# Optimization experiments

Measured on AMD Instinct MI355X. Metric: run time of the kernel, lower is better.

The kernel has to match this reference:

```python
import jax, jax.numpy as jnp
import numpy as np

SCALING = 16.0 / 16.0  # lora_alpha / r

def setup_inputs() -> dict:
    key = jax.random.key(0)
    k1, k2, k3, k4, k5 = jax.random.split(key, 5)
    B, S, D, R = 4, 4096, 4096, 16
    x = jax.random.normal(k1, (B, S, D), dtype=jnp.float32)
    W = jax.random.normal(k2, (D, D), dtype=jnp.float32) * (1.0 / np.sqrt(D))
    bias = jax.random.normal(k3, (D,), dtype=jnp.float32) * 0.02
    lora_A = jax.random.normal(k4, (D, R), dtype=jnp.float32) * (1.0 / np.sqrt(D))
    lora_B = jax.random.normal(k5, (R, D), dtype=jnp.float32) * 0.02
    return {"x": x, "W": W, "bias": bias, "lora_A": lora_A, "lora_B": lora_B}

def reference(x, W, bias, lora_A, lora_B):
    x_dtype = x.dtype
    # base (quantized) linear modeled as dense GEMM: [B,S,D] @ [D,D]
    out = jnp.einsum('bsd,df->bsf', x, W)
    # low-rank LoRA path: (x @ A) @ B * scaling, computed in train_dtype then cast back
    lora = jnp.einsum('bsr,rf->bsf', jnp.einsum('bsd,dr->bsr', x.astype(lora_A.dtype), lora_A), lora_B) * SCALING
    out = out + lora.astype(x_dtype)
    out = out + bias.astype(x_dtype)
    return out
```

## Files before the change

kernel.cpp:

```cpp
#include <hip/hip_runtime.h>
#include <hip/hip_bf16.h>


typedef __attribute__((ext_vector_type(8))) __bf16 bf16x8;
typedef __attribute__((ext_vector_type(4))) float f32x4;

#define M_DIM 16384
#define N_DIM 4096
#define K_DIM 4096

__device__ __forceinline__ void async16(const void* g, void* l) {
    __builtin_amdgcn_global_load_lds((const __attribute__((address_space(1))) void*)g,
                                     (__attribute__((address_space(3))) void*)l,
                                     16, 0, 0);
}

__global__ void cast_x_kernel(const float* __restrict__ x, __bf16* __restrict__ xb, size_t n) {
    size_t i0 = ((size_t)blockIdx.x * blockDim.x + threadIdx.x) * 8;
    size_t stride = (size_t)gridDim.x * blockDim.x * 8;
    for (size_t i = i0; i < n; i += stride) {
        f32x4 v0 = __builtin_nontemporal_load((const f32x4*)(x + i));
        f32x4 v1 = __builtin_nontemporal_load((const f32x4*)(x + i + 4));
        bf16x8 o;
        o[0] = (__bf16)v0[0]; o[1] = (__bf16)v0[1]; o[2] = (__bf16)v0[2]; o[3] = (__bf16)v0[3];
        o[4] = (__bf16)v1[0]; o[5] = (__bf16)v1[1]; o[6] = (__bf16)v1[2]; o[7] = (__bf16)v1[3];
        *(bf16x8*)(xb + i) = o;
    }
}

__global__ void prep_w_kernel(const float* __restrict__ W, const float* __restrict__ A,
                              const float* __restrict__ Bm, __bf16* __restrict__ Wt) {
    __shared__ float Ws[32][33];
    __shared__ float As[32][16];
    __shared__ float Bs[16][32];
    const int tx = threadIdx.x;
    const int ty = threadIdx.y;
    const int t = ty * 32 + tx;
    const int n0 = blockIdx.x * 32;
    const int k0 = blockIdx.y * 32;

#pragma unroll
    for (int i = 0; i < 4; ++i) {
        int k = ty + i * 8;
        Ws[k][tx] = W[(size_t)(k0 + k) * N_DIM + n0 + tx];
    }
    for (int i = t; i < 512; i += 256)
        As[i >> 4][i & 15] = A[(size_t)(k0 + (i >> 4)) * 16 + (i & 15)];
    for (int i = t; i < 512; i += 256)
        Bs[i >> 5][i & 31] = Bm[(size_t)(i >> 5) * N_DIM + n0 + (i & 31)];
    __syncthreads();

    float a[16];
#pragma unroll
    for (int r = 0; r < 16; ++r) a[r] = As[tx][r];
#pragma unroll
    for (int i = 0; i < 4; ++i) {
        int n = ty + i * 8;
        float acc = Ws[tx][n];
#pragma unroll
        for (int r = 0; r < 16; ++r) acc += a[r] * Bs[r][n];
        Wt[(size_t)(n0 + n) * K_DIM + k0 + tx] = (__bf16)acc;
    }
}


#define WAIT_VM(N) asm volatile("s_waitcnt vmcnt(" #N ")" ::: "memory")
#define BARRIER() do { asm volatile("" ::: "memory"); __builtin_amdgcn_s_barrier(); asm volatile("" ::: "memory"); } while (0)

#define STAGE_A(ldsbase, row0, kt) do {                                              \
    int r_ = (row0) + srow;                                                          \
    async16(Xb + (size_t)(m0 + r_) * K_DIM + (kt) + scol,                            \
            (ldsbase) + (row0) * 128 + sldsoff); } while (0)

#define STAGE_B(ldsbase, row0, kt) do {                                              \
    int p_ = (row0) + srow;                                                          \
    int nl_ = ((p_ >> 5) & 3) * 64 + ((p_ >> 7) & 1) * 32 + (p_ & 31);               \
    async16(Wt + (size_t)(n0 + nl_) * K_DIM + (kt) + scol,                           \
            (ldsbase) + (row0) * 128 + sldsoff); } while (0)

#define LOAD_AF(ldsbase, MH)                                                         \
    _Pragma("unroll") for (int m_ = 0; m_ < 4; ++m_)                                 \
    _Pragma("unroll") for (int ks_ = 0; ks_ < 2; ++ks_)                              \
        afr[m_][ks_] = *(const bf16x8*)((ldsbase) + aRowB + (MH) * 8192 + m_ * 2048 + colsw[ks_]);

#define LOAD_BF(dst, ldsbase, NH)                                                    \
    _Pragma("unroll") for (int n_ = 0; n_ < 2; ++n_)                                 \
    _Pragma("unroll") for (int ks_ = 0; ks_ < 2; ++ks_)                              \
        dst[n_][ks_] = *(const bf16x8*)((ldsbase) + bRowB + (NH) * 16384 + n_ * 2048 + colsw[ks_]);

#define MFMA32(MH)                                                                   \
    __builtin_amdgcn_s_setprio(1);                                                   \
    _Pragma("unroll") for (int ks_ = 0; ks_ < 2; ++ks_)                              \
    _Pragma("unroll") for (int m_ = 0; m_ < 4; ++m_) {                               \
        _Pragma("unroll") for (int n_ = 0; n_ < 2; ++n_)                             \
            acc[(MH) * 4 + m_][n_] = __builtin_amdgcn_mfma_f32_16x16x32_bf16(        \
                afr[m_][ks_], b0f[n_][ks_], acc[(MH) * 4 + m_][n_], 0, 0, 0);        \
        _Pragma("unroll") for (int n_ = 0; n_ < 2; ++n_)                             \
            acc[(MH) * 4 + m_][2 + n_] = __builtin_amdgcn_mfma_f32_16x16x32_bf16(    \
                afr[m_][ks_], b1f[n_][ks_], acc[(MH) * 4 + m_][2 + n_], 0, 0, 0);    \
    }                                                                                \
    __builtin_amdgcn_s_setprio(0);                                                   \
    __builtin_amdgcn_sched_barrier(0);

#define PH0(AC, BC, AO, KT)                                                          \
    LOAD_AF(AC, 0);                                                                  \
    LOAD_BF(b0f, BC, 0); LOAD_BF(b1f, BC, 1);                                        \
    STAGE_A(AO, 0, (KT) + 64);  STAGE_A(AO, 128, (KT) + 64);                         \
    STAGE_A(AO, 64, (KT) + 64); STAGE_A(AO, 192, (KT) + 64);                         \
    BARRIER(); MFMA32(0); BARRIER();

#define PH1(AC, BC, KT)                                                              \
    LOAD_AF(AC, 1);                                                                  \
    STAGE_B(BC, 0, (KT) + 128);   STAGE_B(BC, 64, (KT) + 128);                       \
    STAGE_B(BC, 128, (KT) + 128); STAGE_B(BC, 192, (KT) + 128);                      \
    BARRIER(); MFMA32(1); WAIT_VM(4); BARRIER();

__global__ __launch_bounds__(512, 2) void gemm256_kernel(
    const __bf16* __restrict__ Xb, const __bf16* __restrict__ Wt,
    const float* __restrict__ bias, float* __restrict__ out) {
    extern __shared__ __align__(16) char smem[];
    const int tid  = threadIdx.x;
    const int lane = tid & 63;
    const int wave = tid >> 6;
    const int wr = wave >> 2;
    const int wn = wave & 3;

    const int bid = blockIdx.x;
    const int wg = (bid & 7) * 128 + (bid >> 3);
    const int m0 = (wg >> 4) * 256;
    const int n0 = (wg & 15) * 256;

    char* A0 = smem;
    char* B0 = smem + 32768;
    char* A1 = smem + 65536;
    char* B1 = smem + 98304;

    const int srow = tid >> 3;
    const int scol = ((tid & 7) ^ (srow & 7)) << 3;
    const int sldsoff = wave * 1024;

    int colsw[2];
#pragma unroll
    for (int ks = 0; ks < 2; ++ks)
        colsw[ks] = ((ks * 32 + (lane >> 4) * 8) ^ ((lane & 7) * 8)) << 1;
    const int aRowB = (wr * 128 + (lane & 15)) * 128;
    const int bRowB = (wn * 32 + (lane & 15)) * 128;

    f32x4 acc[8][4] = {};
    bf16x8 afr[4][2], b0f[2][2], b1f[2][2];

    STAGE_B(B0, 0, 0);   STAGE_B(B0, 64, 0);  STAGE_B(B0, 128, 0); STAGE_B(B0, 192, 0);
    STAGE_A(A0, 0, 0);   STAGE_A(A0, 128, 0); STAGE_A(A0, 64, 0);  STAGE_A(A0, 192, 0);
    STAGE_B(B1, 0, 64);  STAGE_B(B1, 64, 64); STAGE_B(B1, 128, 64); STAGE_B(B1, 192, 64);
    WAIT_VM(4);
    BARRIER();

    for (int it = 0; it < 31; ++it) {
        const int kt = it * 128;
        PH0(A0, B0, A1, kt);       PH1(A0, B0, kt);
        PH0(A1, B1, A0, kt + 64);  PH1(A1, B1, kt + 64);
    }

    PH0(A0, B0, A1, 3968);
    LOAD_AF(A0, 1);
    BARRIER(); MFMA32(1); WAIT_VM(0); BARRIER();

    LOAD_AF(A1, 0);
    LOAD_BF(b0f, B1, 0); LOAD_BF(b1f, B1, 1);
    BARRIER(); MFMA32(0); BARRIER();
    LOAD_AF(A1, 1);
    MFMA32(1);

#pragma unroll
    for (int mh = 0; mh < 2; ++mh)
#pragma unroll
        for (int m = 0; m < 4; ++m) {
            const int gr = m0 + wr * 128 + mh * 64 + m * 16 + (lane >> 4) * 4;
#pragma unroll
            for (int nh = 0; nh < 2; ++nh)
#pragma unroll
                for (int n = 0; n < 2; ++n) {
                    const int gc = n0 + wn * 64 + nh * 32 + n * 16 + (lane & 15);
                    const float bv = bias[gc];
                    const f32x4 a = acc[mh * 4 + m][nh * 2 + n];
#pragma unroll
                    for (int j = 0; j < 4; ++j)
                        __builtin_nontemporal_store(a[j] + bv,
                            &out[(size_t)(gr + j) * N_DIM + gc]);
                }
        }
}

extern "C" void kernel_launch(void* const* d_in, const int* in_sizes, int n_in,
                              void* d_out, int out_size, void* d_ws, size_t ws_size,
                              hipStream_t stream) {
    const float* x    = (const float*)d_in[0];
    const float* W    = (const float*)d_in[1];
    const float* bias = (const float*)d_in[2];
    const float* lA   = (const float*)d_in[3];
    const float* lB   = (const float*)d_in[4];
    float* out = (float*)d_out;

    __bf16* Xb = (__bf16*)d_ws;
    __bf16* Wt = (__bf16*)((char*)d_ws + (size_t)M_DIM * K_DIM * 2);

    cast_x_kernel<<<2048, 256, 0, stream>>>(x, Xb, (size_t)M_DIM * K_DIM);
    prep_w_kernel<<<dim3(N_DIM / 32, K_DIM / 32), dim3(32, 8), 0, stream>>>(W, lA, lB, Wt);

    (void)hipFuncSetAttribute((const void*)gemm256_kernel,
                              hipFuncAttributeMaxDynamicSharedMemorySize, 131072);
    gemm256_kernel<<<1024, 512, 131072, stream>>>(Xb, Wt, bias, out);
}
```

Baseline: 587.6 us.

## Restructure GEMM mainloop to triple-buffered A with one barrier per tile

Replaces the two-phase, double-buffered K loop with a schedule that keeps three A buffers and two B buffers in LDS. Each 64-wide K tile is now a single step: it issues async loads for the next B tile and for the A tile two steps ahead, loads both A halves into separate register sets, runs all MFMAs, then hits one wait and one barrier. The aim is to cut barriers per tile, drop the sched_barrier, and give the global-to-LDS loads more lead time. In exchange, dynamic LDS grows to 160KB per block, and the extra A fragment registers add register pressure that could cause spills.

```diff
diff --git a/kernel.cpp b/kernel.cpp
--- a/kernel.cpp
+++ b/kernel.cpp
@@ -78,42 +78,45 @@
     async16(Wt + (size_t)(n0 + nl_) * K_DIM + (kt) + scol,                           \
             (ldsbase) + (row0) * 128 + sldsoff); } while (0)
 
-#define LOAD_AF(ldsbase, MH)                                                         \
+#define STAGE_A4(AB, KT) do {                                                        \
+    STAGE_A(AB, 0, KT); STAGE_A(AB, 64, KT);                                         \
+    STAGE_A(AB, 128, KT); STAGE_A(AB, 192, KT); } while (0)
+
+#define STAGE_B4(BB, KT) do {                                                        \
+    STAGE_B(BB, 0, KT); STAGE_B(BB, 64, KT);                                         \
+    STAGE_B(BB, 128, KT); STAGE_B(BB, 192, KT); } while (0)
+
+#define LOAD_AF(dst, ldsbase, MH)                                                    \
     _Pragma("unroll") for (int m_ = 0; m_ < 4; ++m_)                                 \
     _Pragma("unroll") for (int ks_ = 0; ks_ < 2; ++ks_)                              \
-        afr[m_][ks_] = *(const bf16x8*)((ldsbase) + aRowB + (MH) * 8192 + m_ * 2048 + colsw[ks_]);
+        dst[m_][ks_] = *(const bf16x8*)((ldsbase) + aRowB + (MH) * 8192 + m_ * 2048 + colsw[ks_]);
 
 #define LOAD_BF(dst, ldsbase, NH)                                                    \
     _Pragma("unroll") for (int n_ = 0; n_ < 2; ++n_)                                 \
     _Pragma("unroll") for (int ks_ = 0; ks_ < 2; ++ks_)                              \
         dst[n_][ks_] = *(const bf16x8*)((ldsbase) + bRowB + (NH) * 16384 + n_ * 2048 + colsw[ks_]);
 
-#define MFMA32(MH)                                                                   \
+#define MFMA32(AFR, MH)                                                              \
     __builtin_amdgcn_s_setprio(1);                                                   \
     _Pragma("unroll") for (int ks_ = 0; ks_ < 2; ++ks_)                              \
     _Pragma("unroll") for (int m_ = 0; m_ < 4; ++m_) {                               \
         _Pragma("unroll") for (int n_ = 0; n_ < 2; ++n_)                             \
             acc[(MH) * 4 + m_][n_] = __builtin_amdgcn_mfma_f32_16x16x32_bf16(        \
-                afr[m_][ks_], b0f[n_][ks_], acc[(MH) * 4 + m_][n_], 0, 0, 0);        \
+                AFR[m_][ks_], b0f[n_][ks_], acc[(MH) * 4 + m_][n_], 0, 0, 0);        \
         _Pragma("unroll") for (int n_ = 0; n_ < 2; ++n_)                             \
             acc[(MH) * 4 + m_][2 + n_] = __builtin_amdgcn_mfma_f32_16x16x32_bf16(    \
-                afr[m_][ks_], b1f[n_][ks_], acc[(MH) * 4 + m_][2 + n_], 0, 0, 0);    \
+                AFR[m_][ks_], b1f[n_][ks_], acc[(MH) * 4 + m_][2 + n_], 0, 0, 0);    \
     }                                                                                \
-    __builtin_amdgcn_s_setprio(0);                                                   \
-    __builtin_amdgcn_sched_barrier(0);
-
-#define PH0(AC, BC, AO, KT)                                                          \
-    LOAD_AF(AC, 0);                                                                  \
-    LOAD_BF(b0f, BC, 0); LOAD_BF(b1f, BC, 1);                                        \
-    STAGE_A(AO, 0, (KT) + 64);  STAGE_A(AO, 128, (KT) + 64);                         \
-    STAGE_A(AO, 64, (KT) + 64); STAGE_A(AO, 192, (KT) + 64);                         \
-    BARRIER(); MFMA32(0); BARRIER();
-
-#define PH1(AC, BC, KT)                                                              \
-    LOAD_AF(AC, 1);                                                                  \
-    STAGE_B(BC, 0, (KT) + 128);   STAGE_B(BC, 64, (KT) + 128);                       \
-    STAGE_B(BC, 128, (KT) + 128); STAGE_B(BC, 192, (KT) + 128);                      \
-    BARRIER(); MFMA32(1); WAIT_VM(4); BARRIER();
+    __builtin_amdgcn_s_setprio(0);
+
+#define TILE_S(Ax, Bx, BS, AS, KT)                                                   \
+    STAGE_B4(BS, (KT) + 64);                                                         \
+    STAGE_A4(AS, (KT) + 128);                                                        \
+    LOAD_AF(afr0, Ax, 0); LOAD_BF(b0f, Bx, 0); LOAD_BF(b1f, Bx, 1);                  \
+    LOAD_AF(afr1, Ax, 1);                                                            \
+    MFMA32(afr0, 0);                                                                 \
+    MFMA32(afr1, 1);                                                                 \
+    WAIT_VM(4); BARRIER();
 
 __global__ __launch_bounds__(512, 2) void gemm256_kernel(
     const __bf16* __restrict__ Xb, const __bf16* __restrict__ Wt,
@@ -131,9 +134,10 @@
     const int n0 = (wg & 15) * 256;
 
     char* A0 = smem;
-    char* B0 = smem + 32768;
-    char* A1 = smem + 65536;
-    char* B1 = smem + 98304;
+    char* A1 = smem + 32768;
+    char* A2 = smem + 65536;
+    char* B0 = smem + 98304;
+    char* B1 = smem + 131072;
 
     const int srow = tid >> 3;
     const int scol = ((tid & 7) ^ (srow & 7)) << 3;
@@ -147,29 +151,50 @@
     const int bRowB = (wn * 32 + (lane & 15)) * 128;
 
     f32x4 acc[8][4] = {};
-    bf16x8 afr[4][2], b0f[2][2], b1f[2][2];
-
-    STAGE_B(B0, 0, 0);   STAGE_B(B0, 64, 0);  STAGE_B(B0, 128, 0); STAGE_B(B0, 192, 0);
-    STAGE_A(A0, 0, 0);   STAGE_A(A0, 128, 0); STAGE_A(A0, 64, 0);  STAGE_A(A0, 192, 0);
-    STAGE_B(B1, 0, 64);  STAGE_B(B1, 64, 64); STAGE_B(B1, 128, 64); STAGE_B(B1, 192, 64);
-    WAIT_VM(4);
+    bf16x8 afr0[4][2], afr1[4][2], b0f[2][2], b1f[2][2];
+
+    STAGE_B4(B0, 0);
+    STAGE_A4(A0, 0);
+    STAGE_B4(B1, 64);
+    STAGE_A4(A1, 64);
+    WAIT_VM(8);
     BARRIER();
 
-    for (int it = 0; it < 31; ++it) {
-        const int kt = it * 128;
-        PH0(A0, B0, A1, kt);       PH1(A0, B0, kt);
-        PH0(A1, B1, A0, kt + 64);  PH1(A1, B1, kt + 64);
-    }
-
-    PH0(A0, B0, A1, 3968);
-    LOAD_AF(A0, 1);
-    BARRIER(); MFMA32(1); WAIT_VM(0); BARRIER();
-
-    LOAD_AF(A1, 0);
-    LOAD_BF(b0f, B1, 0); LOAD_BF(b1f, B1, 1);
-    BARRIER(); MFMA32(0); BARRIER();
-    LOAD_AF(A1, 1);
-    MFMA32(1);
+    {
+        STAGE_A4(A2, 128);
+        LOAD_AF(afr0, A0, 0); LOAD_BF(b0f, B0, 0); LOAD_BF(b1f, B0, 1);
+        LOAD_AF(afr1, A0, 1);
+        MFMA32(afr0, 0);
+        MFMA32(afr1, 1);
+        WAIT_VM(4); BARRIER();
+    }
+
+    for (int i = 0; i < 10; ++i) {
+        const int kt = 64 + i * 384;
+        TILE_S(A1, B1, B0, A0, kt);
+        TILE_S(A2, B0, B1, A1, kt + 64);
+        TILE_S(A0, B1, B0, A2, kt + 128);
+        TILE_S(A1, B0, B1, A0, kt + 192);
+        TILE_S(A2, B1, B0, A1, kt + 256);
+        TILE_S(A0, B0, B1, A2, kt + 320);
+    }
+    TILE_S(A1, B1, B0, A0, 3904);
+
+    {
+        STAGE_B4(B1, 4032);
+        LOAD_AF(afr0, A2, 0); LOAD_BF(b0f, B0, 0); LOAD_BF(b1f, B0, 1);
+        LOAD_AF(afr1, A2, 1);
+        MFMA32(afr0, 0);
+        MFMA32(afr1, 1);
+        WAIT_VM(0); BARRIER();
+    }
+
+    {
+        LOAD_AF(afr0, A0, 0); LOAD_BF(b0f, B1, 0); LOAD_BF(b1f, B1, 1);
+        LOAD_AF(afr1, A0, 1);
+        MFMA32(afr0, 0);
+        MFMA32(afr1, 1);
+    }
 
 #pragma unroll
     for (int mh = 0; mh < 2; ++mh)
@@ -208,6 +233,6 @@
     prep_w_kernel<<<dim3(N_DIM / 32, K_DIM / 32), dim3(32, 8), 0, stream>>>(W, lA, lB, Wt);
 
     (void)hipFuncSetAttribute((const void*)gemm256_kernel,
-                              hipFuncAttributeMaxDynamicSharedMemorySize, 131072);
-    gemm256_kernel<<<1024, 512, 131072, stream>>>(Xb, Wt, bias, out);
-}
+                              hipFuncAttributeMaxDynamicSharedMemorySize, 163840);
+    gemm256_kernel<<<1024, 512, 163840, stream>>>(Xb, Wt, bias, out);
+}
```

Measured after the change: 693.7 us. 1.18x slower.

## Restructure GEMM main loop into three-barrier tile schedule with split staging

Applied to the files above, without the earlier changes.

Replaces the two-phase-per-tile loop (four barriers per K tile) with a schedule that loads all A and B fragments for a tile up front, then interleaves quarter-sized MFMA groups with staggered async global-to-LDS stores split across half-tiles, using three barriers per tile. Global pointers for each staged row group are precomputed outside the loop to cut address arithmetic. The aim is fewer barriers and better overlap of memory staging with MFMA. The cost is higher register pressure from holding two A fragment sets, which matters under launch_bounds(512,2), and tighter reasoning about LDS buffer reuse hazards.

```diff
diff --git a/kernel.cpp b/kernel.cpp
--- a/kernel.cpp
+++ b/kernel.cpp
@@ -67,53 +67,44 @@
 #define WAIT_VM(N) asm volatile("s_waitcnt vmcnt(" #N ")" ::: "memory")
 #define BARRIER() do { asm volatile("" ::: "memory"); __builtin_amdgcn_s_barrier(); asm volatile("" ::: "memory"); } while (0)
 
-#define STAGE_A(ldsbase, row0, kt) do {                                              \
-    int r_ = (row0) + srow;                                                          \
-    async16(Xb + (size_t)(m0 + r_) * K_DIM + (kt) + scol,                            \
-            (ldsbase) + (row0) * 128 + sldsoff); } while (0)
-
-#define STAGE_B(ldsbase, row0, kt) do {                                              \
-    int p_ = (row0) + srow;                                                          \
-    int nl_ = ((p_ >> 5) & 3) * 64 + ((p_ >> 7) & 1) * 32 + (p_ & 31);               \
-    async16(Wt + (size_t)(n0 + nl_) * K_DIM + (kt) + scol,                           \
-            (ldsbase) + (row0) * 128 + sldsoff); } while (0)
-
-#define LOAD_AF(ldsbase, MH)                                                         \
+#define ST(ptr, koff, ldsbase, row0) \
+    async16((ptr) + (koff), (ldsbase) + (row0) * 128 + sldsoff)
+
+#define LOAD_AF(dst, ldsbase, MH)                                                    \
     _Pragma("unroll") for (int m_ = 0; m_ < 4; ++m_)                                 \
     _Pragma("unroll") for (int ks_ = 0; ks_ < 2; ++ks_)                              \
-        afr[m_][ks_] = *(const bf16x8*)((ldsbase) + aRowB + (MH) * 8192 + m_ * 2048 + colsw[ks_]);
+        dst[m_][ks_] = *(const bf16x8*)((ldsbase) + aRowB + (MH) * 8192 + m_ * 2048 + colsw[ks_]);
 
 #define LOAD_BF(dst, ldsbase, NH)                                                    \
     _Pragma("unroll") for (int n_ = 0; n_ < 2; ++n_)                                 \
     _Pragma("unroll") for (int ks_ = 0; ks_ < 2; ++ks_)                              \
         dst[n_][ks_] = *(const bf16x8*)((ldsbase) + bRowB + (NH) * 16384 + n_ * 2048 + colsw[ks_]);
 
-#define MFMA32(MH)                                                                   \
+#define UPFRONT(AC, BC)                                                              \
+    LOAD_AF(afr0, AC, 0); LOAD_BF(b0f, BC, 0); LOAD_BF(b1f, BC, 1); LOAD_AF(afr1, AC, 1);
+
+#define MFMA_Q(AF, MB, NB, BF)                                                       \
     __builtin_amdgcn_s_setprio(1);                                                   \
     _Pragma("unroll") for (int ks_ = 0; ks_ < 2; ++ks_)                              \
-    _Pragma("unroll") for (int m_ = 0; m_ < 4; ++m_) {                               \
-        _Pragma("unroll") for (int n_ = 0; n_ < 2; ++n_)                             \
-            acc[(MH) * 4 + m_][n_] = __builtin_amdgcn_mfma_f32_16x16x32_bf16(        \
-                afr[m_][ks_], b0f[n_][ks_], acc[(MH) * 4 + m_][n_], 0, 0, 0);        \
-        _Pragma("unroll") for (int n_ = 0; n_ < 2; ++n_)                             \
-            acc[(MH) * 4 + m_][2 + n_] = __builtin_amdgcn_mfma_f32_16x16x32_bf16(    \
-                afr[m_][ks_], b1f[n_][ks_], acc[(MH) * 4 + m_][2 + n_], 0, 0, 0);    \
-    }                                                                                \
-    __builtin_amdgcn_s_setprio(0);                                                   \
-    __builtin_amdgcn_sched_barrier(0);
-
-#define PH0(AC, BC, AO, KT)                                                          \
-    LOAD_AF(AC, 0);                                                                  \
-    LOAD_BF(b0f, BC, 0); LOAD_BF(b1f, BC, 1);                                        \
-    STAGE_A(AO, 0, (KT) + 64);  STAGE_A(AO, 128, (KT) + 64);                         \
-    STAGE_A(AO, 64, (KT) + 64); STAGE_A(AO, 192, (KT) + 64);                         \
-    BARRIER(); MFMA32(0); BARRIER();
-
-#define PH1(AC, BC, KT)                                                              \
-    LOAD_AF(AC, 1);                                                                  \
-    STAGE_B(BC, 0, (KT) + 128);   STAGE_B(BC, 64, (KT) + 128);                       \
-    STAGE_B(BC, 128, (KT) + 128); STAGE_B(BC, 192, (KT) + 128);                      \
-    BARRIER(); MFMA32(1); WAIT_VM(4); BARRIER();
+    _Pragma("unroll") for (int m_ = 0; m_ < 4; ++m_)                                 \
+    _Pragma("unroll") for (int n_ = 0; n_ < 2; ++n_)                                 \
+        acc[(MB) + m_][(NB) + n_] = __builtin_amdgcn_mfma_f32_16x16x32_bf16(         \
+            AF[m_][ks_], BF[n_][ks_], acc[(MB) + m_][(NB) + n_], 0, 0, 0);           \
+    __builtin_amdgcn_s_setprio(0);
+
+#define TILE3(AC, BC, AO, BO, KB)                                                    \
+    UPFRONT(AC, BC);                                                                 \
+    ST(pA1, (KB) + 64, AO, 64);   ST(pA3, (KB) + 64, AO, 192);                       \
+    ST(pB0, (KB) + 64, BO, 0);    ST(pB1, (KB) + 64, BO, 64);                        \
+    MFMA_Q(afr0, 0, 0, b0f);                                                         \
+    BARRIER();                                                                       \
+    ST(pA0, (KB) + 128, AC, 0);   ST(pA2, (KB) + 128, AC, 128);                      \
+    MFMA_Q(afr0, 0, 2, b1f);                                                         \
+    BARRIER();                                                                       \
+    ST(pB2, (KB) + 128, BC, 128); ST(pB3, (KB) + 128, BC, 192);                      \
+    MFMA_Q(afr1, 4, 2, b1f);                                                         \
+    MFMA_Q(afr1, 4, 0, b0f);                                                         \
+    WAIT_VM(4); BARRIER();
 
 __global__ __launch_bounds__(512, 2) void gemm256_kernel(
     const __bf16* __restrict__ Xb, const __bf16* __restrict__ Wt,
@@ -139,6 +130,16 @@
     const int scol = ((tid & 7) ^ (srow & 7)) << 3;
     const int sldsoff = wave * 1024;
 
+    const __bf16* pA0 = Xb + (size_t)(m0 + 0   + srow) * K_DIM + scol;
+    const __bf16* pA1 = Xb + (size_t)(m0 + 64  + srow) * K_DIM + scol;
+    const __bf16* pA2 = Xb + (size_t)(m0 + 128 + srow) * K_DIM + scol;
+    const __bf16* pA3 = Xb + (size_t)(m0 + 192 + srow) * K_DIM + scol;
+#define BPERM(P) ((((P) >> 5) & 3) * 64 + (((P) >> 7) & 1) * 32 + ((P) & 31))
+    const __bf16* pB0 = Wt + (size_t)(n0 + BPERM(0   + srow)) * K_DIM + scol;
+    const __bf16* pB1 = Wt + (size_t)(n0 + BPERM(64  + srow)) * K_DIM + scol;
+    const __bf16* pB2 = Wt + (size_t)(n0 + BPERM(128 + srow)) * K_DIM + scol;
+    const __bf16* pB3 = Wt + (size_t)(n0 + BPERM(192 + srow)) * K_DIM + scol;
+
     int colsw[2];
 #pragma unroll
     for (int ks = 0; ks < 2; ++ks)
@@ -147,29 +148,38 @@
     const int bRowB = (wn * 32 + (lane & 15)) * 128;
 
     f32x4 acc[8][4] = {};
-    bf16x8 afr[4][2], b0f[2][2], b1f[2][2];
-
-    STAGE_B(B0, 0, 0);   STAGE_B(B0, 64, 0);  STAGE_B(B0, 128, 0); STAGE_B(B0, 192, 0);
-    STAGE_A(A0, 0, 0);   STAGE_A(A0, 128, 0); STAGE_A(A0, 64, 0);  STAGE_A(A0, 192, 0);
-    STAGE_B(B1, 0, 64);  STAGE_B(B1, 64, 64); STAGE_B(B1, 128, 64); STAGE_B(B1, 192, 64);
+    bf16x8 afr0[4][2], afr1[4][2], b0f[2][2], b1f[2][2];
+
+    ST(pA0, 0, A0, 0);   ST(pA2, 0, A0, 128);
+    ST(pA1, 0, A0, 64);  ST(pA3, 0, A0, 192);
+    ST(pB0, 0, B0, 0);   ST(pB1, 0, B0, 64);
+    ST(pB2, 0, B0, 128); ST(pB3, 0, B0, 192);
+    ST(pA0, 64, A1, 0);  ST(pA2, 64, A1, 128);
+    ST(pB2, 64, B1, 128); ST(pB3, 64, B1, 192);
     WAIT_VM(4);
     BARRIER();
 
+    int kb = 0;
     for (int it = 0; it < 31; ++it) {
-        const int kt = it * 128;
-        PH0(A0, B0, A1, kt);       PH1(A0, B0, kt);
-        PH0(A1, B1, A0, kt + 64);  PH1(A1, B1, kt + 64);
-    }
-
-    PH0(A0, B0, A1, 3968);
-    LOAD_AF(A0, 1);
-    BARRIER(); MFMA32(1); WAIT_VM(0); BARRIER();
-
-    LOAD_AF(A1, 0);
-    LOAD_BF(b0f, B1, 0); LOAD_BF(b1f, B1, 1);
-    BARRIER(); MFMA32(0); BARRIER();
-    LOAD_AF(A1, 1);
-    MFMA32(1);
+        TILE3(A0, B0, A1, B1, kb);
+        TILE3(A1, B1, A0, B0, kb + 64);
+        kb += 128;
+    }
+
+    UPFRONT(A0, B0);
+    ST(pA1, 4032, A1, 64); ST(pA3, 4032, A1, 192);
+    ST(pB0, 4032, B1, 0);  ST(pB1, 4032, B1, 64);
+    MFMA_Q(afr0, 0, 0, b0f);
+    MFMA_Q(afr0, 0, 2, b1f);
+    MFMA_Q(afr1, 4, 2, b1f);
+    MFMA_Q(afr1, 4, 0, b0f);
+    WAIT_VM(0); BARRIER();
+
+    UPFRONT(A1, B1);
+    MFMA_Q(afr0, 0, 0, b0f);
+    MFMA_Q(afr0, 0, 2, b1f);
+    MFMA_Q(afr1, 4, 2, b1f);
+    MFMA_Q(afr1, 4, 0, b0f);
 
 #pragma unroll
     for (int mh = 0; mh < 2; ++mh)
```

New measurement: 985.0 us. +67.6%, slower.
